# Kernel tuning notes

Measured on AMD Instinct MI355X. Metric: run time of the kernel, lower is better.

Reference implementation:

```python
import jax, jax.numpy as jnp
import numpy as np

EPS = 1e-5  # torch LayerNorm default


def _layer_norm(x, w, b):
    # normalized_shape = [C, K, K] -> normalize over last 3 dims
    m = jnp.mean(x, axis=(-3, -2, -1), keepdims=True)
    v = jnp.var(x, axis=(-3, -2, -1), keepdims=True)
    return (x - m) * jax.lax.rsqrt(v + EPS) * w + b


def setup_inputs() -> dict:
    key = jax.random.key(0)
    k0, k1, k2, k3, k4, k5 = jax.random.split(key, 6)
    B, C, H, W, K = 32, 192, 56, 56, 7
    x = jax.random.normal(k0, (B, C, H, W), jnp.float32)
    ln0_w = jax.random.normal(k1, (C, K, K), jnp.float32)
    ln0_b = jax.random.normal(k2, (C, K, K), jnp.float32)
    conv0_w = jax.random.normal(k3, (C, 1, K, K), jnp.float32) * 0.1
    ln1_w = jax.random.normal(k4, (C, K, K), jnp.float32)
    ln1_b = jax.random.normal(k5, (C, K, K), jnp.float32)
    return {"x": x, "ln0_w": ln0_w, "ln0_b": ln0_b, "conv0_w": conv0_w,
            "ln1_w": ln1_w, "ln1_b": ln1_b}


def reference(x, ln0_w, ln0_b, conv0_w, ln1_w, ln1_b):
    B, C, H, W = x.shape
    K = conv0_w.shape[-1]
    # AdaptiveAvgPool2d((K,K)); H,W divisible by K -> uniform average pooling
    p = x.reshape(B, C, K, H // K, K, W // K).mean(axis=(3, 5))  # [B,C,K,K]
    p = _layer_norm(p, ln0_w, ln0_b)
    # depthwise KxK conv on KxK map, padding 'same'
    p = jax.lax.conv_general_dilated(
        p, conv0_w, window_strides=(1, 1), padding='SAME',
        dimension_numbers=('NCHW', 'OIHW', 'NCHW'), feature_group_count=C)
    p = jax.nn.relu(_layer_norm(p, ln1_w, ln1_b))  # [B,C,K,K] dynamic kernels
    # per-sample, per-channel depthwise conv: fold batch into channels
    ker = p.reshape(B * C, 1, K, K)
    out = jax.lax.conv_general_dilated(
        x.reshape(1, B * C, H, W), ker, window_strides=(1, 1), padding='SAME',
        dimension_numbers=('NCHW', 'OIHW', 'NCHW'), feature_group_count=B * C)
    return out.reshape(B, C, H, W)
```

## Files before the change

### kernel.cpp

```cpp
#include <hip/hip_runtime.h>

#define BB 32
#define CC 192
#define HH 56
#define WW 56
#define KS 7
#define HW 3136
#define KK 49
#define CKK 9408
#define PL 8
#define NCELL (BB * CC * KK)
#define NBC (BB * CC)
#define P0BLK 37
#define MIDBLK 24
#define TABW 56
#define XP 2048

typedef _Float16 h2 __attribute__((ext_vector_type(2)));

__device__ __forceinline__ unsigned int pack16(float a, float b) {
    return __builtin_bit_cast(unsigned int, __builtin_amdgcn_cvt_pkrtz(a, b));
}

__global__ __launch_bounds__(256) void pool_kernel(const float* __restrict__ x,
                                                   float* __restrict__ p0,
                                                   float2* __restrict__ part0,
                                                   unsigned int* __restrict__ x16) {
    __shared__ float red[8];
    int b = blockIdx.x / P0BLK;
    int t = blockIdx.x - b * P0BLK;
    int cell = t * 256 + threadIdx.x;
    float v = 0.f;
    if (cell < CKK) {
        int c = cell / KK;
        int r = cell - c * KK;
        int i = r / KS;
        int j = r - i * KS;
        int bc = b * CC + c;
        const float* src = x + (size_t)bc * HW + (i * PL) * WW + j * PL;
        unsigned int* xp = x16 + (size_t)bc * XP;
        uint4 z = make_uint4(0u, 0u, 0u, 0u);
        float s = 0.f;
#pragma unroll
        for (int p = 0; p < 4; ++p) {
            float4 aA = *(const float4*)(src + (2 * p) * WW);
            float4 aB = *(const float4*)(src + (2 * p) * WW + 4);
            float4 bA = *(const float4*)(src + (2 * p + 1) * WW);
            float4 bB = *(const float4*)(src + (2 * p + 1) * WW + 4);
            s += aA.x + aA.y + aA.z + aA.w + aB.x + aB.y + aB.z + aB.w
               + bA.x + bA.y + bA.z + bA.w + bB.x + bB.y + bB.z + bB.w;
            int pr2 = 4 * i + p + 2;
            *(uint4*)(xp + pr2 * 64 + 4 + 8 * j) =
                make_uint4(pack16(aA.x, bA.x), pack16(aA.y, bA.y),
                           pack16(aA.z, bA.z), pack16(aA.w, bA.w));
            *(uint4*)(xp + pr2 * 64 + 8 + 8 * j) =
                make_uint4(pack16(aB.x, bB.x), pack16(aB.y, bB.y),
                           pack16(aB.z, bB.z), pack16(aB.w, bB.w));
        }
        v = s * (1.f / 64.f);
        p0[b * CKK + cell] = v;

        if (i == 0) {
            *(uint4*)(xp + 0 * 64 + 4 + 8 * j) = z;
            *(uint4*)(xp + 0 * 64 + 8 + 8 * j) = z;
            *(uint4*)(xp + 1 * 64 + 4 + 8 * j) = z;
            *(uint4*)(xp + 1 * 64 + 8 + 8 * j) = z;
        }
        if (i == 6) {
            *(uint4*)(xp + 30 * 64 + 4 + 8 * j) = z;
            *(uint4*)(xp + 30 * 64 + 8 + 8 * j) = z;
            *(uint4*)(xp + 31 * 64 + 4 + 8 * j) = z;
            *(uint4*)(xp + 31 * 64 + 8 + 8 * j) = z;
        }
        if (j == 0) {
#pragma unroll
            for (int p = 0; p < 4; ++p) *(uint4*)(xp + (4 * i + p + 2) * 64) = z;
            if (i == 0) { *(uint4*)(xp + 0) = z;        *(uint4*)(xp + 64) = z; }
            if (i == 6) { *(uint4*)(xp + 30 * 64) = z;  *(uint4*)(xp + 31 * 64) = z; }
        }
        if (j == 6) {
#pragma unroll
            for (int p = 0; p < 4; ++p) *(uint4*)(xp + (4 * i + p + 2) * 64 + 60) = z;
            if (i == 0) { *(uint4*)(xp + 60) = z;           *(uint4*)(xp + 64 + 60) = z; }
            if (i == 6) { *(uint4*)(xp + 30 * 64 + 60) = z; *(uint4*)(xp + 31 * 64 + 60) = z; }
        }
    }
    float sv = v, sq = v * v;
#pragma unroll
    for (int o = 32; o > 0; o >>= 1) {
        sv += __shfl_down(sv, o, 64);
        sq += __shfl_down(sq, o, 64);
    }
    if ((threadIdx.x & 63) == 0) {
        red[(threadIdx.x >> 6) * 2 + 0] = sv;
        red[(threadIdx.x >> 6) * 2 + 1] = sq;
    }
    __syncthreads();
    if (threadIdx.x == 0)
        part0[blockIdx.x] = make_float2(red[0] + red[2] + red[4] + red[6],
                                        red[1] + red[3] + red[5] + red[7]);
}

__global__ __launch_bounds__(512) void mid_kernel(
    const float* __restrict__ p0,
    const float* __restrict__ ln0w, const float* __restrict__ ln0b,
    const float* __restrict__ w0,
    const float2* __restrict__ part0,
    float* __restrict__ q1,
    float2* __restrict__ part1)
{
    __shared__ float red[16];
    int tid  = threadIdx.x;
    int lane = tid & 63;
    int bc   = blockIdx.x * 8 + (tid >> 6);
    int b = bc / CC;
    int c = bc - b * CC;

    float s0 = 0.f, ss0 = 0.f;
    if (lane < P0BLK) {
        float2 p = part0[b * P0BLK + lane];
        s0 = p.x; ss0 = p.y;
    }
#pragma unroll
    for (int o = 32; o > 0; o >>= 1) {
        s0  += __shfl_down(s0, o, 64);
        ss0 += __shfl_down(ss0, o, 64);
    }
    s0  = __shfl(s0, 0, 64);
    ss0 = __shfl(ss0, 0, 64);
    float mean = s0 * (1.f / CKK);
    float rstd = rsqrtf(ss0 * (1.f / CKK) - mean * mean + 1e-5f);

    float val = 0.f;
    if (lane < KK)
        val = (p0[bc * KK + lane] - mean) * rstd * ln0w[c * KK + lane]
              + ln0b[c * KK + lane];

    int i0 = lane / KS;
    int j0 = lane - i0 * KS;
    const float* wc = w0 + c * KK;

    float acc = 0.f;
#pragma unroll
    for (int u = 0; u < KS; ++u) {
        int ii = i0 + u - 3;
#pragma unroll
        for (int v = 0; v < KS; ++v) {
            int jj = j0 + v - 3;
            bool ok = (ii >= 0) && (ii < KS) && (jj >= 0) && (jj < KS);
            int sl = ok ? (ii * KS + jj) : 0;
            float sv = __shfl(val, sl, 64);
            acc += ok ? sv * wc[u * KS + v] : 0.f;
        }
    }
    if (lane >= KK) acc = 0.f;
    if (lane < KK) q1[bc * KK + lane] = acc;

    float s2 = acc, ss2 = acc * acc;
#pragma unroll
    for (int o = 32; o > 0; o >>= 1) {
        s2  += __shfl_down(s2, o, 64);
        ss2 += __shfl_down(ss2, o, 64);
    }
    if (lane == 0) {
        red[(tid >> 6) * 2 + 0] = s2;
        red[(tid >> 6) * 2 + 1] = ss2;
    }
    __syncthreads();
    if (tid == 0) {
        float a = 0.f, q = 0.f;
#pragma unroll
        for (int w = 0; w < 8; ++w) { a += red[2 * w]; q += red[2 * w + 1]; }
        part1[blockIdx.x] = make_float2(a, q);
    }
}

__global__ __launch_bounds__(256) void tab_kernel(
    const float* __restrict__ q1, const float2* __restrict__ part1,
    const float* __restrict__ ln1w, const float* __restrict__ ln1b,
    unsigned int* __restrict__ ktab)
{
    int lane = threadIdx.x & 63;
    int bc   = blockIdx.x * 4 + (threadIdx.x >> 6);
    int b = bc / CC;
    int c = bc - b * CC;

    float s1 = 0.f, ss1 = 0.f;
    if (lane < MIDBLK) {
        float2 p = part1[b * MIDBLK + lane];
        s1 = p.x; ss1 = p.y;
    }
#pragma unroll
    for (int o = 32; o > 0; o >>= 1) {
        s1  += __shfl_down(s1, o, 64);
        ss1 += __shfl_down(ss1, o, 64);
    }
    s1  = __shfl(s1, 0, 64);
    ss1 = __shfl(ss1, 0, 64);
    float m = s1 * (1.f / CKK);
    float r = rsqrtf(ss1 * (1.f / CKK) - m * m + 1e-5f);

    float kt = 0.f;
    if (lane < KK) {
        float v = (q1[(size_t)bc * KK + lane] - m) * r * ln1w[c * KK + lane]
                  + ln1b[c * KK + lane];
        kt = v > 0.f ? v : 0.f;
    }

    bool isDt = lane < 28;
    int idx = isDt ? lane : (lane < TABW ? lane - 28 : 0);
    int e = idx / KS, v = idx - KS * e;
    int iA, iB; bool mA, mB;
    if (isDt) { mA = (e > 0); iA = mA ? (2 * e - 1) * KS + v : 0;
                mB = true;    iB = 2 * e * KS + v; }
    else      { mA = true;    iA = 2 * e * KS + v;
                mB = (e < 3); iB = mB ? (2 * e + 1) * KS + v : 0; }
    float va = __shfl(kt, iA, 64);
    float vb = __shfl(kt, iB, 64);
    unsigned int w = pack16(mA ? va : 0.f, mB ? vb : 0.f);
    if (lane < TABW)
        ktab[(size_t)bc * TABW + lane] = w;
}

__global__ __launch_bounds__(256) void conv_kernel(
    const unsigned int* __restrict__ x16,
    const unsigned int* __restrict__ ktab,
    float* __restrict__ out)
{
    int bc   = blockIdx.x;
    int tid  = threadIdx.x;
    int lane = tid & 63;
    int wid  = tid >> 6;

    const uint4* tb = (const uint4*)(ktab + (size_t)bc * TABW);
    unsigned int dt[28], ct[28];
#pragma unroll
    for (int i = 0; i < 7; ++i) {
        uint4 t4 = tb[i];
        dt[4 * i + 0] = t4.x; dt[4 * i + 1] = t4.y;
        dt[4 * i + 2] = t4.z; dt[4 * i + 3] = t4.w;
    }
#pragma unroll
    for (int i = 0; i < 7; ++i) {
        uint4 t4 = tb[7 + i];
        ct[4 * i + 0] = t4.x; ct[4 * i + 1] = t4.y;
        ct[4 * i + 2] = t4.z; ct[4 * i + 3] = t4.w;
    }

    int ll = lane < 56 ? lane : 55;
    const unsigned int* base = x16 + (size_t)bc * XP + (wid * 7) * 64 + ll + 1;

    float accL[7], accH[7];
#pragma unroll
    for (int t = 0; t < 7; ++t) { accL[t] = 0.f; accH[t] = 0.f; }

    unsigned int wa[KS], wb[KS];
#pragma unroll
    for (int j = 0; j < KS; ++j) wa[j] = base[j];

#define H2(u) __builtin_bit_cast(h2, (u))
#define CONV_STEP(S, CUR)                                                     \
    {                                                                         \
        _Pragma("unroll")                                                     \
        for (int e = 0; e < 4; ++e) {                                         \
            int tl = (S) - e;                                                 \
            if (tl >= 0 && tl <= 6) {                                         \
                _Pragma("unroll")                                             \
                for (int vv = 0; vv < KS; ++vv)                               \
                    accL[tl] = __builtin_amdgcn_fdot2(H2(CUR[vv]),            \
                                   H2(dt[e * KS + vv]), accL[tl], false);     \
            }                                                                 \
            int th = (S) - 1 - e;                                             \
            if (th >= 0 && th <= 6) {                                         \
                _Pragma("unroll")                                             \
                for (int vv = 0; vv < KS; ++vv)                               \
                    accH[th] = __builtin_amdgcn_fdot2(H2(CUR[vv]),            \
                                   H2(ct[e * KS + vv]), accH[th], false);     \
            }                                                                 \
        }                                                                     \
    }

#pragma unroll
    for (int ss = 0; ss < 5; ++ss) {
        int s0 = 2 * ss, s1 = 2 * ss + 1;
        {
            const unsigned int* np = base + s1 * 64;
#pragma unroll
            for (int j = 0; j < KS; ++j) wb[j] = np[j];
        }
        CONV_STEP(s0, wa);
        {
            const unsigned int* np = base + (s0 + 2) * 64;
#pragma unroll
            for (int j = 0; j < KS; ++j) wa[j] = np[j];
        }
        CONV_STEP(s1, wb);
    }
    CONV_STEP(10, wa);
#undef CONV_STEP
#undef H2

    if (lane < WW) {
        float* ob = out + (size_t)bc * HW + (wid * 14) * WW + lane;
#pragma unroll
        for (int t = 0; t < 7; ++t) {
            ob[(2 * t) * WW]     = accL[t];
            ob[(2 * t + 1) * WW] = accH[t];
        }
    }
}

extern "C" void kernel_launch(void* const* d_in, const int* in_sizes, int n_in,
                              void* d_out, int out_size, void* d_ws, size_t ws_size,
                              hipStream_t stream) {
    const float* x    = (const float*)d_in[0];
    const float* ln0w = (const float*)d_in[1];
    const float* ln0b = (const float*)d_in[2];
    const float* w0   = (const float*)d_in[3];
    const float* ln1w = (const float*)d_in[4];
    const float* ln1b = (const float*)d_in[5];
    float* out = (float*)d_out;

    float*  p0    = (float*)d_ws;
    float*  q1    = p0 + NCELL;
    float2* part0 = (float2*)(q1 + NCELL);
    float2* part1 = part0 + BB * P0BLK;
    unsigned int* ktab = (unsigned int*)(part1 + BB * MIDBLK);
    unsigned int* x16  = ktab + (size_t)NBC * TABW;

    pool_kernel<<<BB * P0BLK, 256, 0, stream>>>(x, p0, part0, x16);
    mid_kernel <<<BB * MIDBLK, 512, 0, stream>>>(p0, ln0w, ln0b, w0, part0, q1, part1);
    tab_kernel <<<NBC / 4, 256, 0, stream>>>(q1, part1, ln1w, ln1b, ktab);
    conv_kernel<<<NBC, 256, 0, stream>>>(x16, ktab, out);
}
```

Before: 66.73 us.

## Remap pool kernel to one wavefront per channel plane with coalesced column loads

The pool kernel now assigns one 64-lane wavefront to each (batch, channel) plane. Each lane reads one column down eight rows at a time, giving coalesced row loads and stores of the packed fp16 row pairs, replacing the earlier per-cell strided float4 access. Pooled sums come from xor shuffles, and per-plane partial statistics are written without shared memory or a block sync. The mid kernel then sums 192 per-channel partials per batch. Loads are narrower (scalar instead of float4), and eight of the 64 lanes sit idle.

```diff
diff --git a/kernel.cpp b/kernel.cpp
--- a/kernel.cpp
+++ b/kernel.cpp
@@ -8,10 +8,8 @@
 #define HW 3136
 #define KK 49
 #define CKK 9408
-#define PL 8
 #define NCELL (BB * CC * KK)
 #define NBC (BB * CC)
-#define P0BLK 37
 #define MIDBLK 24
 #define TABW 56
 #define XP 2048
@@ -24,88 +22,67 @@
 
 __global__ __launch_bounds__(256) void pool_kernel(const float* __restrict__ x,
                                                    float* __restrict__ p0,
-                                                   float2* __restrict__ part0,
+                                                   float2* __restrict__ part0c,
                                                    unsigned int* __restrict__ x16) {
-    __shared__ float red[8];
-    int b = blockIdx.x / P0BLK;
-    int t = blockIdx.x - b * P0BLK;
-    int cell = t * 256 + threadIdx.x;
-    float v = 0.f;
-    if (cell < CKK) {
-        int c = cell / KK;
-        int r = cell - c * KK;
-        int i = r / KS;
-        int j = r - i * KS;
-        int bc = b * CC + c;
-        const float* src = x + (size_t)bc * HW + (i * PL) * WW + j * PL;
-        unsigned int* xp = x16 + (size_t)bc * XP;
-        uint4 z = make_uint4(0u, 0u, 0u, 0u);
-        float s = 0.f;
+    int lane = threadIdx.x & 63;
+    int bc   = blockIdx.x * 4 + (threadIdx.x >> 6);
+    const float* src = x + (size_t)bc * HW;
+    unsigned int* xp = x16 + (size_t)bc * XP;
+    bool act = lane < WW;
+    int cl   = act ? lane : WW - 1;
+
+    float sv = 0.f, sq = 0.f;
+#pragma unroll
+    for (int i = 0; i < 7; ++i) {
+        float v[8];
+#pragma unroll
+        for (int r = 0; r < 8; ++r)
+            v[r] = src[(8 * i + r) * WW + cl];
+
 #pragma unroll
         for (int p = 0; p < 4; ++p) {
-            float4 aA = *(const float4*)(src + (2 * p) * WW);
-            float4 aB = *(const float4*)(src + (2 * p) * WW + 4);
-            float4 bA = *(const float4*)(src + (2 * p + 1) * WW);
-            float4 bB = *(const float4*)(src + (2 * p + 1) * WW + 4);
-            s += aA.x + aA.y + aA.z + aA.w + aB.x + aB.y + aB.z + aB.w
-               + bA.x + bA.y + bA.z + bA.w + bB.x + bB.y + bB.z + bB.w;
-            int pr2 = 4 * i + p + 2;
-            *(uint4*)(xp + pr2 * 64 + 4 + 8 * j) =
-                make_uint4(pack16(aA.x, bA.x), pack16(aA.y, bA.y),
-                           pack16(aA.z, bA.z), pack16(aA.w, bA.w));
-            *(uint4*)(xp + pr2 * 64 + 8 + 8 * j) =
-                make_uint4(pack16(aB.x, bB.x), pack16(aB.y, bB.y),
-                           pack16(aB.z, bB.z), pack16(aB.w, bB.w));
-        }
-        v = s * (1.f / 64.f);
-        p0[b * CKK + cell] = v;
-
-        if (i == 0) {
-            *(uint4*)(xp + 0 * 64 + 4 + 8 * j) = z;
-            *(uint4*)(xp + 0 * 64 + 8 + 8 * j) = z;
-            *(uint4*)(xp + 1 * 64 + 4 + 8 * j) = z;
-            *(uint4*)(xp + 1 * 64 + 8 + 8 * j) = z;
-        }
-        if (i == 6) {
-            *(uint4*)(xp + 30 * 64 + 4 + 8 * j) = z;
-            *(uint4*)(xp + 30 * 64 + 8 + 8 * j) = z;
-            *(uint4*)(xp + 31 * 64 + 4 + 8 * j) = z;
-            *(uint4*)(xp + 31 * 64 + 8 + 8 * j) = z;
-        }
-        if (j == 0) {
-#pragma unroll
-            for (int p = 0; p < 4; ++p) *(uint4*)(xp + (4 * i + p + 2) * 64) = z;
-            if (i == 0) { *(uint4*)(xp + 0) = z;        *(uint4*)(xp + 64) = z; }
-            if (i == 6) { *(uint4*)(xp + 30 * 64) = z;  *(uint4*)(xp + 31 * 64) = z; }
-        }
-        if (j == 6) {
-#pragma unroll
-            for (int p = 0; p < 4; ++p) *(uint4*)(xp + (4 * i + p + 2) * 64 + 60) = z;
-            if (i == 0) { *(uint4*)(xp + 60) = z;           *(uint4*)(xp + 64 + 60) = z; }
-            if (i == 6) { *(uint4*)(xp + 30 * 64 + 60) = z; *(uint4*)(xp + 31 * 64 + 60) = z; }
-        }
-    }
-    float sv = v, sq = v * v;
+            unsigned int w = pack16(v[2 * p], v[2 * p + 1]);
+            if (act) xp[(4 * i + p + 2) * 64 + 4 + lane] = w;
+        }
+
+        float cs = ((v[0] + v[1]) + (v[2] + v[3])) + ((v[4] + v[5]) + (v[6] + v[7]));
+        cs += __shfl_xor(cs, 1, 64);
+        cs += __shfl_xor(cs, 2, 64);
+        cs += __shfl_xor(cs, 4, 64);
+        if (act && (lane & 7) == 0) {
+            float pv = cs * (1.f / 64.f);
+            p0[(size_t)bc * KK + i * KS + (lane >> 3)] = pv;
+            sv += pv; sq += pv * pv;
+        }
+    }
+
+    xp[0 * 64 + lane]  = 0u;
+    xp[1 * 64 + lane]  = 0u;
+    xp[30 * 64 + lane] = 0u;
+    xp[31 * 64 + lane] = 0u;
+#pragma unroll
+    for (int t = 0; t < 4; ++t) {
+        int idx = t * 64 + lane;
+        if (idx < 224) {
+            int pr2 = 2 + (idx >> 3);
+            int j = idx & 7;
+            xp[pr2 * 64 + (j < 4 ? j : 56 + j)] = 0u;
+        }
+    }
+
 #pragma unroll
     for (int o = 32; o > 0; o >>= 1) {
         sv += __shfl_down(sv, o, 64);
         sq += __shfl_down(sq, o, 64);
     }
-    if ((threadIdx.x & 63) == 0) {
-        red[(threadIdx.x >> 6) * 2 + 0] = sv;
-        red[(threadIdx.x >> 6) * 2 + 1] = sq;
-    }
-    __syncthreads();
-    if (threadIdx.x == 0)
-        part0[blockIdx.x] = make_float2(red[0] + red[2] + red[4] + red[6],
-                                        red[1] + red[3] + red[5] + red[7]);
+    if (lane == 0) part0c[bc] = make_float2(sv, sq);
 }
 
 __global__ __launch_bounds__(512) void mid_kernel(
     const float* __restrict__ p0,
     const float* __restrict__ ln0w, const float* __restrict__ ln0b,
     const float* __restrict__ w0,
-    const float2* __restrict__ part0,
+    const float2* __restrict__ part0c,
     float* __restrict__ q1,
     float2* __restrict__ part1)
 {
@@ -117,9 +94,10 @@
     int c = bc - b * CC;
 
     float s0 = 0.f, ss0 = 0.f;
-    if (lane < P0BLK) {
-        float2 p = part0[b * P0BLK + lane];
-        s0 = p.x; ss0 = p.y;
+#pragma unroll
+    for (int t = 0; t < 3; ++t) {
+        float2 p = part0c[b * CC + lane + 64 * t];
+        s0 += p.x; ss0 += p.y;
     }
 #pragma unroll
     for (int o = 32; o > 0; o >>= 1) {
@@ -133,7 +111,7 @@
 
     float val = 0.f;
     if (lane < KK)
-        val = (p0[bc * KK + lane] - mean) * rstd * ln0w[c * KK + lane]
+        val = (p0[(size_t)bc * KK + lane] - mean) * rstd * ln0w[c * KK + lane]
               + ln0b[c * KK + lane];
 
     int i0 = lane / KS;
@@ -154,7 +132,7 @@
         }
     }
     if (lane >= KK) acc = 0.f;
-    if (lane < KK) q1[bc * KK + lane] = acc;
+    if (lane < KK) q1[(size_t)bc * KK + lane] = acc;
 
     float s2 = acc, ss2 = acc * acc;
 #pragma unroll
@@ -321,15 +299,15 @@
     const float* ln1b = (const float*)d_in[5];
     float* out = (float*)d_out;
 
-    float*  p0    = (float*)d_ws;
-    float*  q1    = p0 + NCELL;
-    float2* part0 = (float2*)(q1 + NCELL);
-    float2* part1 = part0 + BB * P0BLK;
+    float*  p0     = (float*)d_ws;
+    float*  q1     = p0 + NCELL;
+    float2* part0c = (float2*)(q1 + NCELL);
+    float2* part1  = part0c + NBC;
     unsigned int* ktab = (unsigned int*)(part1 + BB * MIDBLK);
     unsigned int* x16  = ktab + (size_t)NBC * TABW;
 
-    pool_kernel<<<BB * P0BLK, 256, 0, stream>>>(x, p0, part0, x16);
-    mid_kernel <<<BB * MIDBLK, 512, 0, stream>>>(p0, ln0w, ln0b, w0, part0, q1, part1);
+    pool_kernel<<<NBC / 4, 256, 0, stream>>>(x, p0, part0c, x16);
+    mid_kernel <<<BB * MIDBLK, 512, 0, stream>>>(p0, ln0w, ln0b, w0, part0c, q1, part1);
     tab_kernel <<<NBC / 4, 256, 0, stream>>>(q1, part1, ln1w, ln1b, ktab);
     conv_kernel<<<NBC, 256, 0, stream>>>(x16, ktab, out);
 }
```

After: 67.02 us. No clear change (+0.4%).
